# Kernel tuning notes

Measured on AMD Instinct MI355X. Metric: run time of the kernel, lower is better.

The kernel has to match this reference:

```python
import jax, jax.numpy as jnp
import numpy as np

N = 100000       # num nodes
E = 1600000      # num edges (avg degree 16)
IN_DIM = 256
EMB_DIM = 128
K = 2            # nlayers: number of propagation steps


def setup_inputs() -> dict:
    key = jax.random.key(0)
    k1, k2, k3, k4, k5 = jax.random.split(key, 5)
    x = jax.random.normal(k1, (N, IN_DIM), dtype=jnp.float32)
    # glorot-initialized linear weight + zero bias
    scale = jnp.sqrt(6.0 / (IN_DIM + EMB_DIM))
    W = jax.random.uniform(k2, (IN_DIM, EMB_DIM), minval=-scale, maxval=scale, dtype=jnp.float32)
    b = jnp.zeros((EMB_DIM,), dtype=jnp.float32)
    edge_src = jax.random.randint(k3, (E,), 0, N, dtype=jnp.int32)
    edge_dst = jax.random.randint(k4, (E,), 0, N, dtype=jnp.int32)
    # normalized-adjacency-like edge weights (positive, ~1/deg scale)
    edge_w = jax.random.uniform(k5, (E,), dtype=jnp.float32) * (1.0 / 16.0)
    return {"x": x, "W": W, "b": b, "edge_src": edge_src, "edge_dst": edge_dst, "edge_w": edge_w}


def reference(x, W, b, edge_src, edge_dst, edge_w):
    # dropout is identity in eval mode; linear + relu
    h = jax.nn.relu(x @ W + b)  # [N, EMB_DIM]
    # k-step sparse propagation: h <- g @ h, g given as COO edge list
    for _ in range(K):
        msg = h[edge_src] * edge_w[:, None]                     # [E, EMB_DIM]
        h = jax.ops.segment_sum(msg, edge_dst, num_segments=N)  # [N, EMB_DIM]
    return h
```

## Files before the change

### kernel.cpp

```cpp
#include <hip/hip_runtime.h>

#define IN_DIM 256
#define EMB 128
#define BKT_SHIFT 9
#define BKT_NODES 512

typedef __attribute__((ext_vector_type(8))) short short8;
typedef __attribute__((ext_vector_type(4))) float f32x4;

__device__ __forceinline__ unsigned short bf16rtne(float f) {
    unsigned int u = __float_as_uint(f);
    return (unsigned short)((u + 0x7fffu + ((u >> 16) & 1u)) >> 16);
}

__device__ __forceinline__ unsigned int packbf2(float lo, float hi) {
    return ((unsigned int)bf16rtne(hi) << 16) | (unsigned int)bf16rtne(lo);
}

__device__ __forceinline__ short8 pack8(float4 f0, float4 f1) {
    union { uint4 u; short8 s; } U;
    asm("v_cvt_pk_bf16_f32 %0, %1, %2" : "=v"(U.u.x) : "v"(f0.x), "v"(f0.y));
    asm("v_cvt_pk_bf16_f32 %0, %1, %2" : "=v"(U.u.y) : "v"(f0.z), "v"(f0.w));
    asm("v_cvt_pk_bf16_f32 %0, %1, %2" : "=v"(U.u.z) : "v"(f1.x), "v"(f1.y));
    asm("v_cvt_pk_bf16_f32 %0, %1, %2" : "=v"(U.u.w) : "v"(f1.z), "v"(f1.w));
    return U.s;
}


__global__ __launch_bounds__(256) void bucket_hist(const int* __restrict__ dst,
                                                   int* __restrict__ ghist, int E) {
    __shared__ int h[256];
    int t = threadIdx.x;
    h[t] = 0;
    __syncthreads();
    int e0 = blockIdx.x * 1024;
    int e1 = min(E, e0 + 1024);
    for (int i = e0 + t; i < e1; i += 256) atomicAdd(&h[dst[i] >> BKT_SHIFT], 1);
    __syncthreads();
    if (h[t]) atomicAdd(&ghist[t], h[t]);
}

__global__ __launch_bounds__(256) void bucket_scan(const int* __restrict__ ghist,
                                                   int* __restrict__ bucket_off,
                                                   int* __restrict__ gcursor,
                                                   int* __restrict__ row_ptr,
                                                   int NB, int N, int E) {
    __shared__ int s[256];
    int t = threadIdx.x;
    int v = (t < NB) ? ghist[t] : 0;
    s[t] = v;
    __syncthreads();
    for (int off = 1; off < 256; off <<= 1) {
        int u = (t >= off) ? s[t - off] : 0;
        __syncthreads();
        s[t] += u;
        __syncthreads();
    }
    int excl = s[t] - v;
    if (t < NB) {
        bucket_off[t] = excl;
        gcursor[t] = excl;
    }
    if (t == 0) {
        bucket_off[NB] = E;
        row_ptr[N] = E;
    }
}


__global__ __launch_bounds__(512) void bin_scatter(const int* __restrict__ src,
                                                   const int* __restrict__ dst,
                                                   const float* __restrict__ w,
                                                   int* __restrict__ gcursor,
                                                   int2* __restrict__ binned, int E) {
    __shared__ int h[256];
    __shared__ int cur[256];
    int t = threadIdx.x;
    if (t < 256) h[t] = 0;
    __syncthreads();
    int e0 = blockIdx.x * 4096;
    int e1 = min(E, e0 + 4096);
    for (int i = e0 + t; i < e1; i += 512) atomicAdd(&h[dst[i] >> BKT_SHIFT], 1);
    __syncthreads();
    if (t < 256) cur[t] = h[t] ? atomicAdd(&gcursor[t], h[t]) : 0;
    __syncthreads();
    for (int i = e0 + t; i < e1; i += 512) {
        int d = dst[i];
        int b = d >> BKT_SHIFT;
        int ld = d & (BKT_NODES - 1);
        int pos = atomicAdd(&cur[b], 1);
        int2 r;
        r.x = src[i] | (ld << 17);
        r.y = __float_as_int(w[i]);
        binned[pos] = r;
    }
}


__global__ __launch_bounds__(1024) void bucket_sort(const int2* __restrict__ binned,
                                                    const int* __restrict__ bucket_off,
                                                    int2* __restrict__ sorted,
                                                    int* __restrict__ row_ptr, int N) {
    __shared__ int cnt[BKT_NODES];
    __shared__ int cur[BKT_NODES];
    __shared__ int scn[BKT_NODES];
    int t = threadIdx.x;
    int b = blockIdx.x;
    int node0 = b << BKT_SHIFT;
    int nn = min(BKT_NODES, N - node0);
    int beg = bucket_off[b];
    int endb = bucket_off[b + 1];
    if (t < BKT_NODES) cnt[t] = 0;
    __syncthreads();
    for (int i = beg + t; i < endb; i += 1024) {
        int ld = ((unsigned int)binned[i].x) >> 17;
        atomicAdd(&cnt[ld], 1);
    }
    __syncthreads();
    int v = 0;
    if (t < BKT_NODES) {
        v = cnt[t];
        scn[t] = v;
    }
    __syncthreads();
    for (int off = 1; off < BKT_NODES; off <<= 1) {
        int u = 0;
        if (t < BKT_NODES && t >= off) u = scn[t - off];
        __syncthreads();
        if (t < BKT_NODES) scn[t] += u;
        __syncthreads();
    }
    if (t < BKT_NODES) {
        int ep = beg + scn[t] - v;
        cur[t] = ep;
        if (t < nn) row_ptr[node0 + t] = ep;
    }
    __syncthreads();
    for (int i = beg + t; i < endb; i += 1024) {
        int2 r = binned[i];
        int ld = ((unsigned int)r.x) >> 17;
        int pos = atomicAdd(&cur[ld], 1);
        r.x &= 0x1FFFF;
        sorted[pos] = r;
    }
}


__global__ __launch_bounds__(256) void wt_cast(const float* __restrict__ W,
                                               unsigned short* __restrict__ wtg) {
    int i = blockIdx.x * 256 + threadIdx.x;
    int c = i & 127;
    int k = i >> 7;
    wtg[c * 256 + k] = bf16rtne(W[(size_t)k * 128 + c]);
}


__global__ __launch_bounds__(256) void gemm_mfma(const float* __restrict__ x,
                                                 const unsigned short* __restrict__ wtg,
                                                 const float* __restrict__ bias,
                                                 unsigned short* __restrict__ hbf, int N) {
    __shared__ float xsf[128][64];
    __shared__ unsigned short wsh[128][64];
    int tid = threadIdx.x;
    int row0 = blockIdx.x * 128;
    int wv = tid >> 6;
    int lane = tid & 63;
    int lr = lane & 15;
    int lg = lane >> 4;
    int wr = wv * 32;
    const float4 zf4 = make_float4(0.f, 0.f, 0.f, 0.f);

    f32x4 acc[2][8];
#pragma unroll
    for (int m = 0; m < 2; ++m)
#pragma unroll
        for (int n = 0; n < 8; ++n) acc[m][n] = (f32x4){0.f, 0.f, 0.f, 0.f};

    int wcol = tid >> 1;
    int wk0 = (tid & 1) * 32;
    const unsigned short* wrow_p = wtg + (size_t)wcol * IN_DIM + wk0;

    for (int kb = 0; kb < IN_DIM; kb += 64) {
#pragma unroll
        for (int j = 0; j < 8; ++j) {
            int cid = tid + 256 * j;
            int r = cid >> 4;
            int c = cid & 15;
            int rr = row0 + r;
            float4 v = (rr < N) ? *(const float4*)(x + (size_t)rr * IN_DIM + kb + c * 4) : zf4;
            *(float4*)&xsf[r][(c ^ (r & 7)) << 2] = v;
        }
#pragma unroll
        for (int j = 0; j < 4; ++j) {
            uint4 v = ((const uint4*)(wrow_p + kb))[j];
            int ko = (wk0 + j * 8) ^ ((wcol & 7) << 3);
            *(uint4*)&wsh[wcol][ko] = v;
        }
        __syncthreads();

        short8 a[2][2];
#pragma unroll
        for (int m = 0; m < 2; ++m)
#pragma unroll
            for (int kk = 0; kk < 2; ++kk) {
                int r = wr + m * 16 + lr;
                int s = r & 7;
                int c0 = kk * 8 + lg * 2;
                float4 f0 = *(const float4*)&xsf[r][(c0 ^ s) << 2];
                float4 f1 = *(const float4*)&xsf[r][((c0 + 1) ^ s) << 2];
                a[m][kk] = pack8(f0, f1);
            }
#pragma unroll
        for (int n = 0; n < 8; ++n) {
            int c = n * 16 + lr;
            int koff0 = (lg * 8) ^ ((c & 7) << 3);
            int koff1 = (32 + lg * 8) ^ ((c & 7) << 3);
            short8 b0 = *(const short8*)&wsh[c][koff0];
            short8 b1 = *(const short8*)&wsh[c][koff1];
            acc[0][n] = __builtin_amdgcn_mfma_f32_16x16x32_bf16(a[0][0], b0, acc[0][n], 0, 0, 0);
            acc[0][n] = __builtin_amdgcn_mfma_f32_16x16x32_bf16(a[0][1], b1, acc[0][n], 0, 0, 0);
            acc[1][n] = __builtin_amdgcn_mfma_f32_16x16x32_bf16(a[1][0], b0, acc[1][n], 0, 0, 0);
            acc[1][n] = __builtin_amdgcn_mfma_f32_16x16x32_bf16(a[1][1], b1, acc[1][n], 0, 0, 0);
        }
        __syncthreads();
    }

#pragma unroll
    for (int n = 0; n < 8; ++n) {
        int c = n * 16 + lr;
        float bv = bias[c];
#pragma unroll
        for (int m = 0; m < 2; ++m) {
#pragma unroll
            for (int j = 0; j < 4; ++j) {
                int r = row0 + wr + m * 16 + lg * 4 + j;
                if (r < N) {
                    float v = fmaxf(acc[m][n][j] + bv, 0.f);
                    hbf[(size_t)r * EMB + c] = bf16rtne(v);
                }
            }
        }
    }
}


template <int OUTBF>
__global__ __launch_bounds__(256) void prop_g(const unsigned int* __restrict__ hin,
                                              void* __restrict__ hout,
                                              const int* __restrict__ rp,
                                              const int2* __restrict__ rec, int N) {
    int wvid = threadIdx.x >> 6;
    int lane = threadIdx.x & 63;
    int node = blockIdx.x * 4 + wvid;
    if (node >= N) return;
    int beg = __builtin_amdgcn_readfirstlane(rp[node]);
    int end = __builtin_amdgcn_readfirstlane(rp[node + 1]);
    float ax = 0.f, ay = 0.f;
    for (int c0 = beg; c0 < end; c0 += 64) {
        int cnt = end - c0;
        if (cnt > 64) cnt = 64;
        int li = lane < cnt ? lane : 0;
        int2 r = rec[c0 + li];
        for (int jb = 0; jb < cnt; jb += 8) {
            int ssrc[8];
            float sw[8];
#pragma unroll
            for (int k = 0; k < 8; ++k) {
                int jj = jb + k;
                int jc = jj < cnt ? jj : 0;
                ssrc[k] = __builtin_amdgcn_readlane(r.x, jc);
                float wv = __uint_as_float((unsigned int)__builtin_amdgcn_readlane(r.y, jc));
                sw[k] = (jj < cnt) ? wv : 0.f;
            }
            unsigned int g[8];
#pragma unroll
            for (int k = 0; k < 8; ++k) g[k] = hin[(size_t)ssrc[k] * 64 + lane];
#pragma unroll
            for (int k = 0; k < 8; ++k) {
                ax = fmaf(sw[k], __uint_as_float(g[k] << 16), ax);
                ay = fmaf(sw[k], __uint_as_float(g[k] & 0xffff0000u), ay);
            }
        }
    }
    if (OUTBF) {
        ((unsigned int*)hout)[(size_t)node * 64 + lane] = packbf2(ax, ay);
    } else {
        float2 o;
        o.x = ax;
        o.y = ay;
        ((float2*)hout)[(size_t)node * 64 + lane] = o;
    }
}


extern "C" void kernel_launch(void* const* d_in, const int* in_sizes, int n_in,
                              void* d_out, int out_size, void* d_ws, size_t ws_size,
                              hipStream_t stream) {
    const float* x = (const float*)d_in[0];
    const float* W = (const float*)d_in[1];
    const float* b = (const float*)d_in[2];
    const int* esrc = (const int*)d_in[3];
    const int* edst = (const int*)d_in[4];
    const float* ew = (const float*)d_in[5];
    int N = in_sizes[0] / IN_DIM;
    int E = in_sizes[3];
    int NB = (N + BKT_NODES - 1) >> BKT_SHIFT;

    char* p = (char*)d_ws;
    auto alloc = [&](size_t bytes) -> void* {
        void* r = (void*)p;
        p += (bytes + 255) & ~(size_t)255;
        return r;
    };
    unsigned short* hbf = (unsigned short*)alloc((size_t)N * EMB * 2);
    unsigned short* h1bf = (unsigned short*)alloc((size_t)N * EMB * 2);
    unsigned short* wtg = (unsigned short*)alloc((size_t)IN_DIM * EMB * 2);
    int* ghist = (int*)alloc(256 * 4);
    int* gcursor = (int*)alloc(256 * 4);
    int* bucket_off = (int*)alloc((size_t)(NB + 1) * 4);
    int* row_ptr = (int*)alloc((size_t)(N + 1) * 4);
    int2* binned = (int2*)alloc((size_t)E * 8);
    int2* sorted = (int2*)alloc((size_t)E * 8);

    hipMemsetAsync(ghist, 0, 256 * 4, stream);
    wt_cast<<<(IN_DIM * EMB) / 256, 256, 0, stream>>>(W, wtg);
    bucket_hist<<<(E + 1023) / 1024, 256, 0, stream>>>(edst, ghist, E);
    bucket_scan<<<1, 256, 0, stream>>>(ghist, bucket_off, gcursor, row_ptr, NB, N, E);
    bin_scatter<<<(E + 4095) / 4096, 512, 0, stream>>>(esrc, edst, ew, gcursor, binned, E);
    bucket_sort<<<NB, 1024, 0, stream>>>(binned, bucket_off, sorted, row_ptr, N);

    gemm_mfma<<<(N + 127) / 128, 256, 0, stream>>>(x, wtg, b, hbf, N);
    prop_g<1><<<(N + 3) / 4, 256, 0, stream>>>((const unsigned int*)hbf, h1bf, row_ptr, sorted, N);
    prop_g<0><<<(N + 3) / 4, 256, 0, stream>>>((const unsigned int*)h1bf, d_out, row_ptr, sorted, N);
}
```

Measured before the change: 256.5 us.

## Pre-cast x to bf16 and stage GEMM tiles via direct global-to-LDS loads

Adds a separate kernel that converts x to bf16 into a workspace buffer. The GEMM then loads both A and B tiles with global_load_lds directly into swizzled shared memory, removing in-register conversion and the register round trip. The aim is to shrink GEMM load traffic and LDS footprint. The trade-off is an extra full pass over x: it is read in fp32 and written in bf16, then read again, which raises total memory traffic.

```diff
diff --git a/kernel.cpp b/kernel.cpp
--- a/kernel.cpp
+++ b/kernel.cpp
@@ -155,20 +155,29 @@
 }
 
 
-__global__ __launch_bounds__(256) void gemm_mfma(const float* __restrict__ x,
+__global__ __launch_bounds__(256) void x_cast(const float* __restrict__ x,
+                                              unsigned short* __restrict__ xb, int total8) {
+    int stride = gridDim.x * 256;
+    for (int i = blockIdx.x * 256 + threadIdx.x; i < total8; i += stride) {
+        const float4* s = (const float4*)(x + (size_t)i * 8);
+        *(short8*)(xb + (size_t)i * 8) = pack8(s[0], s[1]);
+    }
+}
+
+
+__global__ __launch_bounds__(256) void gemm_mfma(const unsigned short* __restrict__ xb,
                                                  const unsigned short* __restrict__ wtg,
                                                  const float* __restrict__ bias,
                                                  unsigned short* __restrict__ hbf, int N) {
-    __shared__ float xsf[128][64];
-    __shared__ unsigned short wsh[128][64];
+    __shared__ unsigned short As[128][64];
+    __shared__ unsigned short Bs[128][64];
     int tid = threadIdx.x;
-    int row0 = blockIdx.x * 128;
     int wv = tid >> 6;
     int lane = tid & 63;
     int lr = lane & 15;
     int lg = lane >> 4;
     int wr = wv * 32;
-    const float4 zf4 = make_float4(0.f, 0.f, 0.f, 0.f);
+    int row0 = blockIdx.x * 128;
 
     f32x4 acc[2][8];
 #pragma unroll
@@ -176,25 +185,27 @@
 #pragma unroll
         for (int n = 0; n < 8; ++n) acc[m][n] = (f32x4){0.f, 0.f, 0.f, 0.f};
 
-    int wcol = tid >> 1;
-    int wk0 = (tid & 1) * 32;
-    const unsigned short* wrow_p = wtg + (size_t)wcol * IN_DIM + wk0;
+    int p0 = wv * 4 * 64 + lane;
 
     for (int kb = 0; kb < IN_DIM; kb += 64) {
 #pragma unroll
-        for (int j = 0; j < 8; ++j) {
-            int cid = tid + 256 * j;
-            int r = cid >> 4;
-            int c = cid & 15;
-            int rr = row0 + r;
-            float4 v = (rr < N) ? *(const float4*)(x + (size_t)rr * IN_DIM + kb + c * 4) : zf4;
-            *(float4*)&xsf[r][(c ^ (r & 7)) << 2] = v;
-        }
-#pragma unroll
-        for (int j = 0; j < 4; ++j) {
-            uint4 v = ((const uint4*)(wrow_p + kb))[j];
-            int ko = (wk0 + j * 8) ^ ((wcol & 7) << 3);
-            *(uint4*)&wsh[wcol][ko] = v;
+        for (int i = 0; i < 4; ++i) {
+            int p = p0 + i * 64;
+            int r = p >> 3;
+            int c = p & 7;
+            int cs = (c ^ (r & 7)) * 8;
+            int gr = row0 + r;
+            if (gr >= N) gr = N - 1;
+            const unsigned short* ga = xb + (size_t)gr * IN_DIM + kb + cs;
+            __builtin_amdgcn_global_load_lds(
+                (const __attribute__((address_space(1))) void*)ga,
+                (__attribute__((address_space(3))) void*)((char*)&As[0][0] + (size_t)(wv * 4 + i) * 1024),
+                16, 0, 0);
+            const unsigned short* gb = wtg + (size_t)r * IN_DIM + kb + cs;
+            __builtin_amdgcn_global_load_lds(
+                (const __attribute__((address_space(1))) void*)gb,
+                (__attribute__((address_space(3))) void*)((char*)&Bs[0][0] + (size_t)(wv * 4 + i) * 1024),
+                16, 0, 0);
         }
         __syncthreads();
 
@@ -204,19 +215,15 @@
 #pragma unroll
             for (int kk = 0; kk < 2; ++kk) {
                 int r = wr + m * 16 + lr;
-                int s = r & 7;
-                int c0 = kk * 8 + lg * 2;
-                float4 f0 = *(const float4*)&xsf[r][(c0 ^ s) << 2];
-                float4 f1 = *(const float4*)&xsf[r][((c0 + 1) ^ s) << 2];
-                a[m][kk] = pack8(f0, f1);
+                int ch = kk * 4 + lg;
+                a[m][kk] = *(const short8*)&As[r][((ch ^ (r & 7)) * 8)];
             }
 #pragma unroll
         for (int n = 0; n < 8; ++n) {
-            int c = n * 16 + lr;
-            int koff0 = (lg * 8) ^ ((c & 7) << 3);
-            int koff1 = (32 + lg * 8) ^ ((c & 7) << 3);
-            short8 b0 = *(const short8*)&wsh[c][koff0];
-            short8 b1 = *(const short8*)&wsh[c][koff1];
+            int cc = n * 16 + lr;
+            int sw = cc & 7;
+            short8 b0 = *(const short8*)&Bs[cc][(((0 * 4 + lg) ^ sw) * 8)];
+            short8 b1 = *(const short8*)&Bs[cc][(((1 * 4 + lg) ^ sw) * 8)];
             acc[0][n] = __builtin_amdgcn_mfma_f32_16x16x32_bf16(a[0][0], b0, acc[0][n], 0, 0, 0);
             acc[0][n] = __builtin_amdgcn_mfma_f32_16x16x32_bf16(a[0][1], b1, acc[0][n], 0, 0, 0);
             acc[1][n] = __builtin_amdgcn_mfma_f32_16x16x32_bf16(a[1][0], b0, acc[1][n], 0, 0, 0);
@@ -315,6 +322,7 @@
     unsigned short* hbf = (unsigned short*)alloc((size_t)N * EMB * 2);
     unsigned short* h1bf = (unsigned short*)alloc((size_t)N * EMB * 2);
     unsigned short* wtg = (unsigned short*)alloc((size_t)IN_DIM * EMB * 2);
+    unsigned short* xbf = (unsigned short*)alloc((size_t)N * IN_DIM * 2);
     int* ghist = (int*)alloc(256 * 4);
     int* gcursor = (int*)alloc(256 * 4);
     int* bucket_off = (int*)alloc((size_t)(NB + 1) * 4);
@@ -324,12 +332,13 @@
 
     hipMemsetAsync(ghist, 0, 256 * 4, stream);
     wt_cast<<<(IN_DIM * EMB) / 256, 256, 0, stream>>>(W, wtg);
+    x_cast<<<2048, 256, 0, stream>>>(x, xbf, N * IN_DIM / 8);
     bucket_hist<<<(E + 1023) / 1024, 256, 0, stream>>>(edst, ghist, E);
     bucket_scan<<<1, 256, 0, stream>>>(ghist, bucket_off, gcursor, row_ptr, NB, N, E);
     bin_scatter<<<(E + 4095) / 4096, 512, 0, stream>>>(esrc, edst, ew, gcursor, binned, E);
     bucket_sort<<<NB, 1024, 0, stream>>>(binned, bucket_off, sorted, row_ptr, N);
 
-    gemm_mfma<<<(N + 127) / 128, 256, 0, stream>>>(x, wtg, b, hbf, N);
+    gemm_mfma<<<(N + 127) / 128, 256, 0, stream>>>(xbf, wtg, b, hbf, N);
     prop_g<1><<<(N + 3) / 4, 256, 0, stream>>>((const unsigned int*)hbf, h1bf, row_ptr, sorted, N);
     prop_g<0><<<(N + 3) / 4, 256, 0, stream>>>((const unsigned int*)h1bf, d_out, row_ptr, sorted, N);
 }
```

Result: slower. 264.0 us (+2.9%).
